# Performance work log

Measured on AMD Instinct MI355X. Metric: run time of the kernel, lower is better.

The kernel has to match this reference:

```python
import jax, jax.numpy as jnp
import numpy as np

CH = 64
CF = CH // 8  # f/g projection channels


def setup_inputs() -> dict:
    key = jax.random.key(0)
    k1, k2, k3, k4, k5 = jax.random.split(key, 5)
    x = jax.random.normal(k1, (8, 64, 64, CH), dtype=jnp.float32)
    kernel_f = 0.02 * jax.random.normal(k2, (1, 1, CH, CF), dtype=jnp.float32)
    kernel_g = 0.02 * jax.random.normal(k3, (1, 1, CH, CF), dtype=jnp.float32)
    kernel_h = 0.02 * jax.random.normal(k4, (1, 1, CH, CH), dtype=jnp.float32)
    gamma = 0.02 * jax.random.normal(k5, (1,), dtype=jnp.float32)
    return {"x": x, "kernel_f": kernel_f, "kernel_g": kernel_g,
            "kernel_h": kernel_h, "gamma": gamma}


def reference(x, kernel_f, kernel_g, kernel_h, gamma):
    B, H, W, C = x.shape
    N = H * W
    xf = x.reshape(B, N, C)  # flatten spatial; 1x1 conv == matmul over channels
    f = jnp.einsum('bnc,cd->bnd', xf, kernel_f[0, 0])  # [B,N,CF]
    g = jnp.einsum('bnc,cd->bnd', xf, kernel_g[0, 0])  # [B,N,CF]
    h = jnp.einsum('bnc,cd->bnd', xf, kernel_h[0, 0])  # [B,N,C]
    s = jnp.einsum('bnd,bmd->bnm', g, f)  # g @ f^T, [B,N,N]
    beta = jax.nn.softmax(s, axis=-1)
    o = jnp.einsum('bnm,bmc->bnc', beta, h)  # [B,N,C]
    out = gamma * o.reshape(B, H, W, C) + x
    return out
```

## Files before the change

### kernel.cpp

```cpp
#include <hip/hip_runtime.h>
#include <hip/hip_bf16.h>

typedef __attribute__((ext_vector_type(4)))  float f32x4;
typedef __attribute__((ext_vector_type(16))) float f32x16;
typedef __attribute__((ext_vector_type(8)))  short bf16x8;

#define LOG2E 1.44269504088896340736f

#if __has_builtin(__builtin_amdgcn_exp2f)
static __device__ __forceinline__ float exp2_native(float x) {
  return __builtin_amdgcn_exp2f(x);
}
#else
extern "C" __device__ float __ocml_native_exp2_f32(float);
static __device__ __forceinline__ float exp2_native(float x) {
  return __ocml_native_exp2_f32(x);
}
#endif

static __device__ __forceinline__ unsigned int pack_trunc_f(float a, float b) {
  return __builtin_amdgcn_perm(__float_as_uint(b), __float_as_uint(a), 0x07060302);
}

typedef const __attribute__((address_space(1))) unsigned int gu32;
typedef __attribute__((address_space(3))) unsigned int lu32;
static __device__ __forceinline__ void gload_lds16(const void* g, void* l) {
  __builtin_amdgcn_global_load_lds((gu32*)g, (lu32*)l, 16, 0, 0);
}

__global__ __launch_bounds__(256) void proj_kernel(
    const float* __restrict__ x, const float* __restrict__ kf,
    const float* __restrict__ kg, const float* __restrict__ kh,
    unsigned short* __restrict__ f_b, unsigned short* __restrict__ g_b,
    unsigned short* __restrict__ h_p)
{
  __shared__ unsigned short Kt[80*72];
  const int t = threadIdx.x;
  const int idb = blockIdx.x;
  const int blk = (idb & 7)*64 + (idb >> 3);

  #pragma unroll
  for (int r = 0; r < 20; ++r) {
    int idx = r*256 + t;
    int o = idx >> 6, c = idx & 63;
    float v = (o < 8) ? kf[c*8 + o]
            : (o < 16) ? kg[c*8 + (o-8)] * LOG2E
            : kh[c*64 + (o-16)];
    Kt[o*72 + c] = (unsigned short)(__float_as_uint(v) >> 16);
  }
  __syncthreads();

  const int w = t >> 6, lane = t & 63, l15 = lane & 15, quad = lane >> 4;
  const int Rbase = blk*64 + w*16;
  const int R = Rbase + l15;

  bf16x8 af[2];
  #pragma unroll
  for (int kk = 0; kk < 2; ++kk) {
    const float* xp = x + (long)R*64 + kk*32 + quad*8;
    float4 v0 = *(const float4*)xp;
    float4 v1 = *(const float4*)(xp + 4);
    union { unsigned int u[4]; bf16x8 v; } p;
    p.u[0] = pack_trunc_f(v0.x, v0.y);
    p.u[1] = pack_trunc_f(v0.z, v0.w);
    p.u[2] = pack_trunc_f(v1.x, v1.y);
    p.u[3] = pack_trunc_f(v1.z, v1.w);
    af[kk] = p.v;
  }

  f32x4 acc[5];
  #pragma unroll
  for (int nt = 0; nt < 5; ++nt) { f32x4 z = {}; acc[nt] = z; }

  #pragma unroll
  for (int nt = 0; nt < 5; ++nt)
    #pragma unroll
    for (int kk = 0; kk < 2; ++kk) {
      bf16x8 bfv = *(const bf16x8*)&Kt[(nt*16 + l15)*72 + kk*32 + quad*8];
      acc[nt] = __builtin_amdgcn_mfma_f32_16x16x32_bf16(af[kk], bfv, acc[nt], 0, 0, 0);
    }

  const int bt = Rbase >> 12;
  const int kt = (Rbase >> 7) & 31;
  const int base = ((blk & 1) << 6) + (w << 4);
  const int pi = base + ((quad & 1) << 3) + (((quad >> 1) & 1) << 2);

  #pragma unroll
  for (int rr = 0; rr < 4; ++rr) {
    const int nq = (Rbase + quad*4 + rr) & 4095;
    unsigned short v = (unsigned short)(__float_as_uint(acc[0][rr]) >> 16);
    if (l15 < 8) f_b[((long)bt*4096 + nq)*8 + l15] = v;
    else         g_b[((long)bt*4096 + nq)*8 + (l15 - 8)] = v;
  }
  #pragma unroll
  for (int nt = 1; nt < 5; ++nt) {
    const int c = (nt - 1)*16 + l15;
    uint2 v;
    v.x = pack_trunc_f(acc[nt][0], acc[nt][1]);
    v.y = pack_trunc_f(acc[nt][2], acc[nt][3]);
    *(uint2*)(h_p + ((long)(bt*32 + kt)*64 + c)*136 + pi) = v;
  }
}

__global__ __launch_bounds__(512, 4) void attn_kernel(
    const unsigned short* __restrict__ f_b, const unsigned short* __restrict__ g_b,
    const unsigned short* __restrict__ h_p,
    const float* __restrict__ x, const float* __restrict__ gamma_p,
    float* __restrict__ out)
{
  extern __shared__ char smem[];

  const int t = threadIdx.x;
  const int w = t >> 6, lane = t & 63, l31 = lane & 31, a = lane >> 5;
  const int qg = w & 1, ks = w >> 1;
  const int id = blockIdx.x;
  const int b = id & 7, qb = id >> 3;
  const int q0 = qb*64 + qg*32;

  bf16x8 gfv;
  {
    bf16x8 gv = *(const bf16x8*)(g_b + ((long)b*4096 + q0 + l31)*8);
    bf16x8 z = {};
    gfv = (a == 0) ? gv : z;
  }
  bf16x8 bhl;
  {
    union { unsigned short s[8]; bf16x8 v; } o8;
    #pragma unroll
    for (int j = 0; j < 8; ++j) o8.s[j] = 0x3F80;
    bf16x8 z = {};
    bhl = (l31 == 0) ? o8.v : z;
  }

  f32x16 oacc[2], ol;
  { f32x16 z = {}; oacc[0] = z; oacc[1] = z; ol = z; }

  const char* hp_b = (const char*)h_p + (long)b*32*17408;
  const char* fb_b = (const char*)f_b + (long)b*4096*16;

  auto stage = [&](int bi, int kt) {
    const char* hsrc = hp_b + (long)kt*17408;
    const char* fsrc = fb_b + (long)kt*2048;
    char* dst = smem + bi*19456;
    #pragma unroll
    for (int i = 0; i < 3; ++i) {
      const int c = i*8 + w;
      if (c < 19) {
        const int off = c*1024;
        const char* src = (off < 17408) ? (hsrc + off) : (fsrc + (off - 17408));
        gload_lds16(src + lane*16, dst + off);
      }
    }
  };

  stage(0, 0);

  for (int ktl = 0; ktl < 32; ++ktl) {
    __syncthreads();
    if (ktl < 31) stage((ktl + 1) & 1, ktl + 1);

    const unsigned short* hts = (const unsigned short*)(smem + (ktl & 1)*19456);
    const unsigned short* fts = hts + 8704;

    bf16x8 afv = *(const bf16x8*)&fts[(ks*32 + l31)*8];
    f32x16 zz = {};
    f32x16 sc = __builtin_amdgcn_mfma_f32_32x32x16_bf16(afv, gfv, zz, 0, 0, 0);

    #pragma unroll
    for (int half = 0; half < 2; ++half) {
      const int s = ks*2 + half;
      bf16x8 bh0 = *(const bf16x8*)&hts[(l31)*136      + s*16 + a*8];
      bf16x8 bh1 = *(const bf16x8*)&hts[(32 + l31)*136 + s*16 + a*8];
      union { unsigned int u[4]; bf16x8 v; } ap;
      #pragma unroll
      for (int j = 0; j < 4; ++j) {
        float ea = exp2_native(sc[half*8 + 2*j]);
        float eb = exp2_native(sc[half*8 + 2*j + 1]);
        ap.u[j] = pack_trunc_f(ea, eb);
      }
      oacc[0] = __builtin_amdgcn_mfma_f32_32x32x16_bf16(ap.v, bh0, oacc[0], 0, 0, 0);
      oacc[1] = __builtin_amdgcn_mfma_f32_32x32x16_bf16(ap.v, bh1, oacc[1], 0, 0, 0);
      ol      = __builtin_amdgcn_mfma_f32_32x32x16_bf16(ap.v, bhl, ol,      0, 0, 0);
    }
  }

  __syncthreads();
  float* cb = (float*)smem;
  #pragma unroll
  for (int sl = 1; sl <= 3; ++sl) {
    if (ks == sl) {
      float* d = cb + (qg*64 + lane)*49;
      #pragma unroll
      for (int r = 0; r < 16; ++r) {
        d[r] = oacc[0][r]; d[16 + r] = oacc[1][r]; d[32 + r] = ol[r];
      }
    }
    __syncthreads();
    if (ks == 0) {
      const float* sp = cb + (qg*64 + lane)*49;
      #pragma unroll
      for (int r = 0; r < 16; ++r) {
        oacc[0][r] += sp[r]; oacc[1][r] += sp[16 + r]; ol[r] += sp[32 + r];
      }
    }
    __syncthreads();
  }

  if (ks == 0) {
    const float gamma = gamma_p[0];
    const float* xb = x + ((long)b*4096 + q0)*64;
    float* ob = out + ((long)b*4096 + q0)*64;

    #pragma unroll
    for (int r = 0; r < 16; ++r) {
      const int q = (r & 3) + 8*(r >> 2) + 4*a;
      const float lq = __shfl(ol[r], lane & 32);
      const float s = gamma / lq;
      #pragma unroll
      for (int nt = 0; nt < 2; ++nt) {
        const long idx = (long)q*64 + nt*32 + l31;
        ob[idx] = fmaf(s, oacc[nt][r], xb[idx]);
      }
    }
  }
}

extern "C" void kernel_launch(void* const* d_in, const int* in_sizes, int n_in,
                              void* d_out, int out_size, void* d_ws, size_t ws_size,
                              hipStream_t stream) {
  const float* x  = (const float*)d_in[0];
  const float* kf = (const float*)d_in[1];
  const float* kg = (const float*)d_in[2];
  const float* kh = (const float*)d_in[3];
  const float* gamma = (const float*)d_in[4];
  float* out = (float*)d_out;

  char* ws = (char*)d_ws;
  unsigned short* h_p = (unsigned short*)ws;
  unsigned short* f_b = (unsigned short*)(ws + 4456448);
  unsigned short* g_b = (unsigned short*)(ws + 4980736);

  proj_kernel<<<512, 256, 0, stream>>>(x, kf, kg, kh, f_b, g_b, h_p);
  attn_kernel<<<512, 512, 38912, stream>>>(f_b, g_b, h_p, x, gamma, out);
}
```

Measured before the change: 104.6 us.

## Double attention block query tile and stage two key tiles per barrier

The attention kernel now uses 1024-thread blocks covering 128 queries, with 4 query groups times 4 key splits. Each block stages two 64-key tiles per double-buffer step, so one K/V load is shared by twice as many queries and there are half as many barriers. The cross-split reduction is reorganised into two rounds that each sum three partial buffers. The cost is more LDS per block (77 KB) and a grid of 256 blocks, which risks lower occupancy and poor tail balance across CUs.

New measurement: 102.9 us. Within noise of the previous version (-1.6%).

```diff
diff --git a/kernel.cpp b/kernel.cpp
--- a/kernel.cpp
+++ b/kernel.cpp
@@ -102,7 +102,7 @@
   }
 }
 
-__global__ __launch_bounds__(512, 4) void attn_kernel(
+__global__ __launch_bounds__(1024, 4) void attn_kernel(
     const unsigned short* __restrict__ f_b, const unsigned short* __restrict__ g_b,
     const unsigned short* __restrict__ h_p,
     const float* __restrict__ x, const float* __restrict__ gamma_p,
@@ -112,10 +112,10 @@
 
   const int t = threadIdx.x;
   const int w = t >> 6, lane = t & 63, l31 = lane & 31, a = lane >> 5;
-  const int qg = w & 1, ks = w >> 1;
+  const int qg = w & 3, ks = w >> 2;
   const int id = blockIdx.x;
   const int b = id & 7, qb = id >> 3;
-  const int q0 = qb*64 + qg*32;
+  const int q0 = qb*128 + qg*32;
 
   bf16x8 gfv;
   {
@@ -138,16 +138,19 @@
   const char* hp_b = (const char*)h_p + (long)b*32*17408;
   const char* fb_b = (const char*)f_b + (long)b*4096*16;
 
-  auto stage = [&](int bi, int kt) {
-    const char* hsrc = hp_b + (long)kt*17408;
-    const char* fsrc = fb_b + (long)kt*2048;
-    char* dst = smem + bi*19456;
+  auto stage = [&](int bi, int tp) {
+    char* dst = smem + bi*38912;
     #pragma unroll
     for (int i = 0; i < 3; ++i) {
-      const int c = i*8 + w;
-      if (c < 19) {
+      const int c = i*16 + w;
+      if (c < 38) {
         const int off = c*1024;
-        const char* src = (off < 17408) ? (hsrc + off) : (fsrc + (off - 17408));
+        const int sub = (off >= 19456);
+        const int kt = tp*2 + sub;
+        const int within = off - sub*19456;
+        const char* src = (within < 17408)
+            ? (hp_b + (long)kt*17408 + within)
+            : (fb_b + (long)kt*2048 + (within - 17408));
         gload_lds16(src + lane*16, dst + off);
       }
     }
@@ -155,52 +158,60 @@
 
   stage(0, 0);
 
-  for (int ktl = 0; ktl < 32; ++ktl) {
+  for (int tp = 0; tp < 16; ++tp) {
     __syncthreads();
-    if (ktl < 31) stage((ktl + 1) & 1, ktl + 1);
-
-    const unsigned short* hts = (const unsigned short*)(smem + (ktl & 1)*19456);
-    const unsigned short* fts = hts + 8704;
-
-    bf16x8 afv = *(const bf16x8*)&fts[(ks*32 + l31)*8];
-    f32x16 zz = {};
-    f32x16 sc = __builtin_amdgcn_mfma_f32_32x32x16_bf16(afv, gfv, zz, 0, 0, 0);
-
-    #pragma unroll
-    for (int half = 0; half < 2; ++half) {
-      const int s = ks*2 + half;
-      bf16x8 bh0 = *(const bf16x8*)&hts[(l31)*136      + s*16 + a*8];
-      bf16x8 bh1 = *(const bf16x8*)&hts[(32 + l31)*136 + s*16 + a*8];
-      union { unsigned int u[4]; bf16x8 v; } ap;
-      #pragma unroll
-      for (int j = 0; j < 4; ++j) {
-        float ea = exp2_native(sc[half*8 + 2*j]);
-        float eb = exp2_native(sc[half*8 + 2*j + 1]);
-        ap.u[j] = pack_trunc_f(ea, eb);
-      }
-      oacc[0] = __builtin_amdgcn_mfma_f32_32x32x16_bf16(ap.v, bh0, oacc[0], 0, 0, 0);
-      oacc[1] = __builtin_amdgcn_mfma_f32_32x32x16_bf16(ap.v, bh1, oacc[1], 0, 0, 0);
-      ol      = __builtin_amdgcn_mfma_f32_32x32x16_bf16(ap.v, bhl, ol,      0, 0, 0);
+    if (tp < 15) stage((tp + 1) & 1, tp + 1);
+
+    const char* bufb = smem + (tp & 1)*38912;
+
+    #pragma unroll
+    for (int sub = 0; sub < 2; ++sub) {
+      const unsigned short* hts = (const unsigned short*)(bufb + sub*19456);
+      const unsigned short* fts = hts + 8704;
+
+      bf16x8 afv = *(const bf16x8*)&fts[(ks*32 + l31)*8];
+      f32x16 zz = {};
+      f32x16 sc = __builtin_amdgcn_mfma_f32_32x32x16_bf16(afv, gfv, zz, 0, 0, 0);
+
+      #pragma unroll
+      for (int half = 0; half < 2; ++half) {
+        const int s = ks*2 + half;
+        bf16x8 bh0 = *(const bf16x8*)&hts[(l31)*136      + s*16 + a*8];
+        bf16x8 bh1 = *(const bf16x8*)&hts[(32 + l31)*136 + s*16 + a*8];
+        union { unsigned int u[4]; bf16x8 v; } ap;
+        #pragma unroll
+        for (int j = 0; j < 4; ++j) {
+          float ea = exp2_native(sc[half*8 + 2*j]);
+          float eb = exp2_native(sc[half*8 + 2*j + 1]);
+          ap.u[j] = pack_trunc_f(ea, eb);
+        }
+        oacc[0] = __builtin_amdgcn_mfma_f32_32x32x16_bf16(ap.v, bh0, oacc[0], 0, 0, 0);
+        oacc[1] = __builtin_amdgcn_mfma_f32_32x32x16_bf16(ap.v, bh1, oacc[1], 0, 0, 0);
+        ol      = __builtin_amdgcn_mfma_f32_32x32x16_bf16(ap.v, bhl, ol,      0, 0, 0);
+      }
     }
   }
 
   __syncthreads();
   float* cb = (float*)smem;
   #pragma unroll
-  for (int sl = 1; sl <= 3; ++sl) {
-    if (ks == sl) {
-      float* d = cb + (qg*64 + lane)*49;
+  for (int rnd = 0; rnd < 2; ++rnd) {
+    if ((qg >> 1) == rnd && ks > 0) {
+      float* d = cb + (((qg & 1)*3 + (ks - 1))*64 + lane)*49;
       #pragma unroll
       for (int r = 0; r < 16; ++r) {
         d[r] = oacc[0][r]; d[16 + r] = oacc[1][r]; d[32 + r] = ol[r];
       }
     }
     __syncthreads();
-    if (ks == 0) {
-      const float* sp = cb + (qg*64 + lane)*49;
-      #pragma unroll
-      for (int r = 0; r < 16; ++r) {
-        oacc[0][r] += sp[r]; oacc[1][r] += sp[16 + r]; ol[r] += sp[32 + r];
+    if ((qg >> 1) == rnd && ks == 0) {
+      #pragma unroll
+      for (int sl = 0; sl < 3; ++sl) {
+        const float* sp = cb + (((qg & 1)*3 + sl)*64 + lane)*49;
+        #pragma unroll
+        for (int r = 0; r < 16; ++r) {
+          oacc[0][r] += sp[r]; oacc[1][r] += sp[16 + r]; ol[r] += sp[32 + r];
+        }
       }
     }
     __syncthreads();
@@ -241,5 +252,5 @@
   unsigned short* g_b = (unsigned short*)(ws + 4980736);
 
   proj_kernel<<<512, 256, 0, stream>>>(x, kf, kg, kh, f_b, g_b, h_p);
-  attn_kernel<<<512, 512, 38912, stream>>>(f_b, g_b, h_p, x, gamma, out);
-}
+  attn_kernel<<<256, 1024, 77824, stream>>>(f_b, g_b, h_p, x, gamma, out);
+}
```
